# Performance work log

Hardware: AMD Instinct MI355X
Metric: run time of the kernel (lower is better)

The kernel has to match this reference:

```python
import jax, jax.numpy as jnp
import numpy as np

V, NLAB, NLAYERS, DI, DM, DS, DD, K = 32000, 9, 2, 768, 1536, 16, 96, 4
B, S = 2, 2048
EPS = 1e-6


def setup_inputs() -> dict:
    key = jax.random.key(0)
    ks = jax.random.split(key, 12)
    n = lambda k, shape, s=0.02: jax.random.normal(k, shape, jnp.float32) * s
    return {
        "input_ids": jax.random.randint(ks[0], (B, S), 0, V, dtype=jnp.int32),
        "attention_mask": jnp.ones((B, S), jnp.int32),
        "emb": n(ks[1], (V, DI)),
        "norm_w": jnp.ones((NLAYERS, DI), jnp.float32),
        "in_proj_w": n(ks[2], (NLAYERS, 2 * DM, DI)),
        "conv_w": n(ks[3], (NLAYERS, DM, K), 0.1),
        "conv_b": jnp.zeros((NLAYERS, DM), jnp.float32),
        "sB_w": n(ks[4], (NLAYERS, DS, DM)),
        "sC_w": n(ks[5], (NLAYERS, DS, DM)),
        "sD1_w": n(ks[6], (NLAYERS, DD, DM)),
        "sD2_w": n(ks[7], (NLAYERS, DM, DD)),
        "A": jnp.tile(jnp.arange(1, DS + 1, dtype=jnp.float32), (NLAYERS, DM, 1)),
        "Dp": jnp.ones((NLAYERS, DM), jnp.float32),
        "out_w": n(ks[8], (NLAYERS, DI, DM)),
        "cls_w": n(ks[9], (NLAB, DI)),
        "cls_b": jnp.zeros((NLAB,), jnp.float32),
    }


def _rmsnorm(x, w):
    return x * jax.lax.rsqrt(jnp.mean(x * x, axis=-1, keepdims=True) + EPS) * w


def _mamba_block(x, norm_w, Wi, cw, cb, WB, WC, W1, W2, A, Dp, Wo):
    # x: (b, l, d_input)
    h = _rmsnorm(x, norm_w)
    a, gate = jnp.split(h @ Wi.T, 2, axis=-1)  # each (b, l, DM)
    # causal depthwise conv1d, kernel K, left-pad K-1 (== Conv1d(pad=K-1)[..., :l])
    L = a.shape[1]
    ap = jnp.pad(a, ((0, 0), (K - 1, 0), (0, 0)))
    conv = cb + sum(ap[:, i:i + L, :] * cw[:, i] for i in range(K))
    a = jax.nn.silu(conv)
    # selective SSM
    Bm = a @ WB.T                                   # (b, l, DS)
    Cm = a @ WC.T                                   # (b, l, DS)
    delta = jax.nn.softplus(Dp + (a @ W1.T) @ W2.T)  # (b, l, DM)
    A_bar = jnp.exp(delta[..., None] * (-A))         # (b, l, DM, DS)
    X_bar = (delta * a)[..., None] * Bm[:, :, None, :]  # (b, l, DM, DS)

    def comb(c1, c2):
        a1, x1 = c1
        a2, x2 = c2
        return a1 * a2, a2 * x1 + x2

    _, hid = jax.lax.associative_scan(comb, (A_bar, X_bar), axis=1)
    y = jnp.einsum('blds,bls->bld', hid, Cm) + Dp * a
    y = y * jax.nn.silu(gate)
    return y @ Wo.T


def _forward(input_ids, attention_mask, emb, norm_w, in_proj_w, conv_w, conv_b,
             sB_w, sC_w, sD1_w, sD2_w, A, Dp, out_w, cls_w, cls_b):
    x = emb[input_ids] * attention_mask[..., None].astype(emb.dtype)
    for i in range(NLAYERS):  # residual Mamba layers
        x = _mamba_block(x, norm_w[i], in_proj_w[i], conv_w[i], conv_b[i],
                         sB_w[i], sC_w[i], sD1_w[i], sD2_w[i], A[i], Dp[i], out_w[i]) + x
    # dropout is identity at inference
    return x @ cls_w.T + cls_b  # logits (b, l, num_labels)


def reference(input_ids, attention_mask, emb, norm_w, in_proj_w, conv_w, conv_b,
              sB_w, sC_w, sD1_w, sD2_w, A, Dp, out_w, cls_w, cls_b):
    return _forward(input_ids, attention_mask, emb, norm_w, in_proj_w, conv_w, conv_b,
                    sB_w, sC_w, sD1_w, sD2_w, A, Dp, out_w, cls_w, cls_b)
```

## Files before the change

### kernel.cpp

```cpp
#include <hip/hip_runtime.h>
#include <hip/hip_bf16.h>
#include <math.h>

#define NLAB 9
#define NL   2
#define DI   768
#define DM   1536
#define DS   16
#define KC   4
#define DD   96
#define BB   2
#define SS   2048
#define TT   (BB*SS)
#define EPSF 1e-6f

#define NCH  64
#define CL   (SS/NCH)

#define NW   128
#define KS   8
#define KSL  (DM/KS)

typedef __attribute__((ext_vector_type(4))) float f32x4;
typedef __attribute__((ext_vector_type(8))) short bf16x8;
typedef __attribute__((ext_vector_type(4))) unsigned short us4;

__device__ __forceinline__ float siluf(float x) { return x / (1.f + __expf(-x)); }
__device__ __forceinline__ float softplusf(float x) { return x > 15.f ? x : log1pf(__expf(x)); }

__device__ __forceinline__ unsigned short f2bf(float f) {
    unsigned u = __float_as_uint(f);
    return (unsigned short)((u + 0x7fffu + ((u >> 16) & 1u)) >> 16);
}

__global__ void f32_to_bf16(const float* __restrict__ src,
                            unsigned short* __restrict__ dst, int n)
{
    int i = (blockIdx.x * 256 + threadIdx.x) * 8;
    if (i >= n) return;
    float4 a = *(const float4*)(src + i);
    float4 b = *(const float4*)(src + i + 4);
    union { unsigned short s[8]; uint4 v; } o;
    o.s[0] = f2bf(a.x); o.s[1] = f2bf(a.y); o.s[2] = f2bf(a.z); o.s[3] = f2bf(a.w);
    o.s[4] = f2bf(b.x); o.s[5] = f2bf(b.y); o.s[6] = f2bf(b.z); o.s[7] = f2bf(b.w);
    *(uint4*)(dst + i) = o.v;
}

__global__ void embed_kernel(const int* __restrict__ ids, const int* __restrict__ mask,
                             const float* __restrict__ emb, float* __restrict__ x)
{
    int t = blockIdx.x;
    int i = threadIdx.x;
    float m = (float)mask[t];
    int id = ids[t];
    float4 v = ((const float4*)(emb + (size_t)id * DI))[i];
    v.x *= m; v.y *= m; v.z *= m; v.w *= m;
    ((float4*)(x + (size_t)t * DI))[i] = v;
}

__global__ void rmsnorm_kernel(const float* __restrict__ x, const float* __restrict__ w,
                               unsigned short* __restrict__ h)
{
    __shared__ float red[4];
    int t = blockIdx.x;
    const float* xr = x + (size_t)t * DI;
    float ss = 0.f;
    for (int i = threadIdx.x; i < DI; i += 256) { float v = xr[i]; ss += v * v; }
    #pragma unroll
    for (int m = 1; m < 64; m <<= 1) ss += __shfl_xor(ss, m, 64);
    if ((threadIdx.x & 63) == 0) red[threadIdx.x >> 6] = ss;
    __syncthreads();
    float scale = rsqrtf((red[0] + red[1] + red[2] + red[3]) * (1.f / DI) + EPSF);
    for (int i = threadIdx.x; i < DI; i += 256)
        h[(size_t)t * DI + i] = f2bf(xr[i] * scale * w[i]);
}

#define STAGE_TILE(AS, BS, KT) do {                                                           \
    _Pragma("unroll")                                                                         \
    for (int it = 0; it < 2; ++it) {                                                          \
        int rbase = it * 64 + wave * 16;                                                      \
        int row = rbase + (lane >> 2);                                                        \
        int c8 = (lane & 3) * 8;                                                              \
        __builtin_amdgcn_global_load_lds(                                                     \
            (const __attribute__((address_space(1))) unsigned int*)(Arow + (size_t)row * lda + (KT) + c8), \
            (__attribute__((address_space(3))) unsigned int*)((AS) + rbase * 32), 16, 0, 0);  \
        __builtin_amdgcn_global_load_lds(                                                     \
            (const __attribute__((address_space(1))) unsigned int*)(Brow + (size_t)row * ldb + (KT) + c8), \
            (__attribute__((address_space(3))) unsigned int*)((BS) + rbase * 32), 16, 0, 0);  \
    } } while (0)

#define COMPUTE_TILE(AS, BS) do {                                                             \
    bf16x8 af[4], bfr[4];                                                                     \
    _Pragma("unroll")                                                                         \
    for (int i = 0; i < 4; ++i)                                                               \
        af[i] = *(const bf16x8*)&(AS)[(wm + i * 16 + lr) * 32 + kh * 8];                      \
    _Pragma("unroll")                                                                         \
    for (int j = 0; j < 4; ++j)                                                               \
        bfr[j] = *(const bf16x8*)&(BS)[(wn + j * 16 + lr) * 32 + kh * 8];                     \
    _Pragma("unroll")                                                                         \
    for (int i = 0; i < 4; ++i)                                                               \
        _Pragma("unroll")                                                                     \
        for (int j = 0; j < 4; ++j)                                                           \
            acc[i][j] = __builtin_amdgcn_mfma_f32_16x16x32_bf16(af[i], bfr[j], acc[i][j], 0, 0, 0); \
    } while (0)

__global__ __launch_bounds__(256) void gemm_bf16(
    const unsigned short* __restrict__ A, const unsigned short* __restrict__ B,
    const float* __restrict__ Rres, const float* __restrict__ bias,
    float* __restrict__ C, int M, int N, int K,
    int lda, int ldb, int ldc, int act, int cstride)
{
    __shared__ unsigned short As0[128 * 32];
    __shared__ unsigned short Bs0[128 * 32];
    __shared__ unsigned short As1[128 * 32];
    __shared__ unsigned short Bs1[128 * 32];
    const int tid = threadIdx.x;
    const int wave = tid >> 6, lane = tid & 63;
    const int bm = blockIdx.y * 128, bn = blockIdx.x * 128;
    const int wm = (wave >> 1) * 64, wn = (wave & 1) * 64;
    const int lr = lane & 15, kh = lane >> 4;

    f32x4 acc[4][4] = {};

    const unsigned short* Arow = A + (size_t)bm * lda;
    const unsigned short* Brow = B + (size_t)bn * ldb;

    STAGE_TILE(As0, Bs0, 0);
    __syncthreads();

    int kt = 0;
    while (true) {
        if (kt + 32 < K) STAGE_TILE(As1, Bs1, kt + 32);
        COMPUTE_TILE(As0, Bs0);
        __syncthreads();
        kt += 32;
        if (kt >= K) break;
        if (kt + 32 < K) STAGE_TILE(As0, Bs0, kt + 32);
        COMPUTE_TILE(As1, Bs1);
        __syncthreads();
        kt += 32;
        if (kt >= K) break;
    }

    #pragma unroll
    for (int i = 0; i < 4; ++i) {
        #pragma unroll
        for (int j = 0; j < 4; ++j) {
            #pragma unroll
            for (int r = 0; r < 4; ++r) {
                int row = bm + wm + i * 16 + kh * 4 + r;
                int col = bn + wn + j * 16 + lr;
                float v = acc[i][j][r];
                if (bias) v += bias[col];
                if (act == 1) v = softplusf(v);
                if (Rres) v += Rres[(size_t)row * ldc + col];
                C[((size_t)row * ldc + col) * cstride] = v;
            }
        }
    }
}

__global__ __launch_bounds__(256) void gemm_skinny_bf16(
    const unsigned short* __restrict__ A, const unsigned short* __restrict__ B,
    float* __restrict__ Part)
{
    __shared__ unsigned short As0[128 * 32];
    __shared__ unsigned short Bs0[128 * 32];
    __shared__ unsigned short As1[128 * 32];
    __shared__ unsigned short Bs1[128 * 32];
    const int tid = threadIdx.x;
    const int wave = tid >> 6, lane = tid & 63;
    const int bm = blockIdx.x * 128;
    const int ks = blockIdx.y;
    const int k0 = ks * KSL;
    const int wm = (wave >> 1) * 64, wn = (wave & 1) * 64;
    const int lr = lane & 15, kh = lane >> 4;
    const int lda = DM, ldb = DM;

    f32x4 acc[4][4] = {};

    const unsigned short* Arow = A + (size_t)bm * DM;
    const unsigned short* Brow = B;

    STAGE_TILE(As0, Bs0, k0);
    __syncthreads();

    int kt = 0;
    while (true) {
        if (kt + 32 < KSL) STAGE_TILE(As1, Bs1, k0 + kt + 32);
        COMPUTE_TILE(As0, Bs0);
        __syncthreads();
        kt += 32;
        if (kt >= KSL) break;
        if (kt + 32 < KSL) STAGE_TILE(As0, Bs0, k0 + kt + 32);
        COMPUTE_TILE(As1, Bs1);
        __syncthreads();
        kt += 32;
        if (kt >= KSL) break;
    }

    float* out = Part + (size_t)ks * TT * NW;
    #pragma unroll
    for (int i = 0; i < 4; ++i) {
        #pragma unroll
        for (int j = 0; j < 4; ++j) {
            #pragma unroll
            for (int r = 0; r < 4; ++r) {
                int row = bm + wm + i * 16 + kh * 4 + r;
                int col = wn + j * 16 + lr;
                out[(size_t)row * NW + col] = acc[i][j][r];
            }
        }
    }
}

__global__ void skinny_reduce(const float* __restrict__ Part,
                              float* __restrict__ BCD, unsigned short* __restrict__ dd16)
{
    int idx = blockIdx.x * 256 + threadIdx.x;
    float s = 0.f;
    #pragma unroll
    for (int ks = 0; ks < KS; ++ks)
        s += Part[(size_t)ks * TT * NW + idx];
    BCD[idx] = s;
    int col = idx & (NW - 1);
    if (col >= 32)
        dd16[(size_t)(idx >> 7) * DD + (col - 32)] = f2bf(s);
}

__global__ void conv_silu_kernel(const float* __restrict__ proj, const float* __restrict__ cw,
                                 const float* __restrict__ cb, float* __restrict__ av,
                                 unsigned short* __restrict__ aconv16)
{
    int t = blockIdx.x;
    int d = blockIdx.y * 256 + threadIdx.x;
    int p = t & (SS - 1);
    float acc = cb[d];
    #pragma unroll
    for (int j = 0; j < KC; ++j) {
        int pp = p - (KC - 1) + j;
        if (pp >= 0)
            acc += cw[d * KC + j] * proj[(size_t)(t - (KC - 1) + j) * (2 * DM) + d];
    }
    float v = siluf(acc);
    av[(size_t)t * DM + d] = v;
    aconv16[(size_t)t * DM + d] = f2bf(v);
}

__global__ void concat_w_kernel(const float* __restrict__ WB, const float* __restrict__ WC,
                                const float* __restrict__ W1, unsigned short* __restrict__ Wcat16)
{
    int l = blockIdx.y;
    int row = blockIdx.x;
    const float* src;
    if (row < 16)      src = WB + (size_t)l * DS * DM + (size_t)row * DM;
    else if (row < 32) src = WC + (size_t)l * DS * DM + (size_t)(row - 16) * DM;
    else               src = W1 + (size_t)l * DD * DM + (size_t)(row - 32) * DM;
    unsigned short* dst = Wcat16 + ((size_t)l * NW + row) * DM;
    for (int i = threadIdx.x; i < DM / 4; i += 256) {
        float4 v = ((const float4*)src)[i];
        us4 u = { f2bf(v.x), f2bf(v.y), f2bf(v.z), f2bf(v.w) };
        *(us4*)(dst + i * 4) = u;
    }
}

__global__ __launch_bounds__(256) void scan_pass1(
    const float* __restrict__ dtv, const float* __restrict__ av,
    const float* __restrict__ BCD, const float* __restrict__ Amat,
    float2* __restrict__ PQ)
{
    __shared__ float4 sB4[CL][DS / 4];
    int b = blockIdx.z, c = blockIdx.y;
    int d = blockIdx.x * 256 + threadIdx.x;
    size_t rowbase = (size_t)b * SS + (size_t)c * CL;

    for (int i = threadIdx.x; i < CL * DS; i += 256)
        ((float*)sB4)[i] = BCD[(rowbase + (i >> 4)) * NW + (i & 15)];
    __syncthreads();

    float negA[DS], hid[DS];
    #pragma unroll
    for (int s = 0; s < DS; ++s) {
        negA[s] = -Amat[(size_t)d * DS + s];
        hid[s] = 0.f;
    }
    float cum = 0.f;

    const float* pd = dtv + rowbase * DM + d;
    const float* pa = av  + rowbase * DM + d;
    for (int t = 0; t < CL; ++t) {
        float dt = pd[(size_t)t * DM];
        float avv = pa[(size_t)t * DM];
        cum += dt;
        float xv = dt * avv;
        #pragma unroll
        for (int j = 0; j < DS / 4; ++j) {
            float4 bv = sB4[t][j];
            hid[4*j+0] = __expf(dt * negA[4*j+0]) * hid[4*j+0] + xv * bv.x;
            hid[4*j+1] = __expf(dt * negA[4*j+1]) * hid[4*j+1] + xv * bv.y;
            hid[4*j+2] = __expf(dt * negA[4*j+2]) * hid[4*j+2] + xv * bv.z;
            hid[4*j+3] = __expf(dt * negA[4*j+3]) * hid[4*j+3] + xv * bv.w;
        }
    }
    float2* out = PQ + ((size_t)(b * NCH + c) * DM + d) * DS;
    #pragma unroll
    for (int s = 0; s < DS; ++s)
        out[s] = make_float2(__expf(cum * negA[s]), hid[s]);
}

__global__ void scan_carry(float2* __restrict__ PQ)
{
    int idx = blockIdx.x * 256 + threadIdx.x;
    int b = idx / (DM * DS);
    int r = idx - b * (DM * DS);
    float carry = 0.f;
    for (int c = 0; c < NCH; ++c) {
        size_t o = (size_t)(b * NCH + c) * (DM * DS) + r;
        float2 pq = PQ[o];
        PQ[o].x = carry;
        carry = pq.x * carry + pq.y;
    }
}

__global__ __launch_bounds__(256) void scan_pass2(
    const float* __restrict__ dtv, const float* __restrict__ av,
    const float* __restrict__ BCD,
    const float* __restrict__ proj, const float* __restrict__ Amat,
    const float* __restrict__ Dp, const float2* __restrict__ PQ,
    unsigned short* __restrict__ y)
{
    __shared__ float4 sB4[CL][DS / 4];
    __shared__ float4 sC4[CL][DS / 4];
    int b = blockIdx.z, c = blockIdx.y;
    int d = blockIdx.x * 256 + threadIdx.x;
    size_t rowbase = (size_t)b * SS + (size_t)c * CL;

    for (int i = threadIdx.x; i < CL * DS; i += 256) {
        size_t row = rowbase + (i >> 4);
        ((float*)sB4)[i] = BCD[row * NW + (i & 15)];
        ((float*)sC4)[i] = BCD[row * NW + 16 + (i & 15)];
    }
    __syncthreads();

    float negA[DS], hid[DS];
    const float2* pin = PQ + ((size_t)(b * NCH + c) * DM + d) * DS;
    #pragma unroll
    for (int s = 0; s < DS; ++s) {
        negA[s] = -Amat[(size_t)d * DS + s];
        hid[s] = pin[s].x;
    }
    float Dpd = Dp[d];

    const float* pd = dtv + rowbase * DM + d;
    const float* pa = av  + rowbase * DM + d;
    const float* gp = proj + rowbase * (2 * DM) + DM + d;
    unsigned short* yp = y + rowbase * DM + d;

    for (int t = 0; t < CL; ++t) {
        float dt = pd[(size_t)t * DM];
        float avv = pa[(size_t)t * DM];
        float g  = gp[(size_t)t * (2 * DM)];
        float xv = dt * avv;
        float acc0 = 0.f, acc1 = 0.f, acc2 = 0.f, acc3 = 0.f;
        #pragma unroll
        for (int j = 0; j < DS / 4; ++j) {
            float4 bv = sB4[t][j];
            float4 cv = sC4[t][j];
            hid[4*j+0] = __expf(dt * negA[4*j+0]) * hid[4*j+0] + xv * bv.x;
            hid[4*j+1] = __expf(dt * negA[4*j+1]) * hid[4*j+1] + xv * bv.y;
            hid[4*j+2] = __expf(dt * negA[4*j+2]) * hid[4*j+2] + xv * bv.z;
            hid[4*j+3] = __expf(dt * negA[4*j+3]) * hid[4*j+3] + xv * bv.w;
            acc0 += hid[4*j+0] * cv.x;
            acc1 += hid[4*j+1] * cv.y;
            acc2 += hid[4*j+2] * cv.z;
            acc3 += hid[4*j+3] * cv.w;
        }
        float contrib = (acc0 + acc1) + (acc2 + acc3);
        yp[(size_t)t * DM] = f2bf((contrib + Dpd * avv) * siluf(g));
    }
}

__global__ void cls_kernel(const float* __restrict__ x, const float* __restrict__ W,
                           const float* __restrict__ bias, float* __restrict__ out)
{
    int t = blockIdx.x;
    int lane = threadIdx.x;
    const float* xr = x + (size_t)t * DI;
    float acc[NLAB];
    #pragma unroll
    for (int n = 0; n < NLAB; ++n) acc[n] = 0.f;
    for (int i = lane; i < DI; i += 64) {
        float xv = xr[i];
        #pragma unroll
        for (int n = 0; n < NLAB; ++n) acc[n] += xv * W[(size_t)n * DI + i];
    }
    #pragma unroll
    for (int n = 0; n < NLAB; ++n)
        #pragma unroll
        for (int m = 1; m < 64; m <<= 1) acc[n] += __shfl_xor(acc[n], m, 64);
    if (lane < NLAB) out[(size_t)t * NLAB + lane] = acc[lane] + bias[lane];
}

extern "C" void kernel_launch(void* const* d_in, const int* in_sizes, int n_in,
                              void* d_out, int out_size, void* d_ws, size_t ws_size,
                              hipStream_t stream)
{
    const int*   ids    = (const int*)d_in[0];
    const int*   mask   = (const int*)d_in[1];
    const float* emb    = (const float*)d_in[2];
    const float* norm_w = (const float*)d_in[3];
    const float* Wi     = (const float*)d_in[4];
    const float* conv_w = (const float*)d_in[5];
    const float* conv_b = (const float*)d_in[6];
    const float* sB_w   = (const float*)d_in[7];
    const float* sC_w   = (const float*)d_in[8];
    const float* sD1_w  = (const float*)d_in[9];
    const float* sD2_w  = (const float*)d_in[10];
    const float* Amat   = (const float*)d_in[11];
    const float* Dp     = (const float*)d_in[12];
    const float* out_w  = (const float*)d_in[13];
    const float* cls_w  = (const float*)d_in[14];
    const float* cls_b  = (const float*)d_in[15];
    float* logits = (float*)d_out;

    float* ws = (float*)d_ws;
    size_t off = 0;
    float* x     = ws + off; off += (size_t)TT * DI;
    float* proj  = ws + off; off += (size_t)TT * 2 * DM;
    float* dtv   = ws + off; off += (size_t)TT * DM;
    float* av    = ws + off; off += (size_t)TT * DM;
    float* BCD   = ws + off; off += (size_t)TT * NW;
    size_t scratch_sz = (size_t)BB * NCH * DM * DS * 2;
    size_t part_sz = (size_t)KS * TT * NW;
    if (part_sz > scratch_sz) scratch_sz = part_sz;
    float* Part  = ws + off;
    float2* PQ   = (float2*)(ws + off); off += scratch_sz;
    unsigned short* y16     = (unsigned short*)(ws + off); off += (size_t)TT * DM / 2;
    unsigned short* aconv16 = (unsigned short*)(ws + off); off += (size_t)TT * DM / 2;
    unsigned short* Wi16    = (unsigned short*)(ws + off); off += (size_t)NL * 2 * DM * DI / 2;
    unsigned short* Wo16    = (unsigned short*)(ws + off); off += (size_t)NL * DI * DM / 2;
    unsigned short* W216    = (unsigned short*)(ws + off); off += (size_t)NL * DM * DD / 2;
    unsigned short* dd16    = (unsigned short*)(ws + off); off += (size_t)TT * DD / 2;
    unsigned short* Wcat16  = (unsigned short*)(ws + off); off += (size_t)NL * NW * DM / 2;
    if (ws_size < off * sizeof(float)) return;

    unsigned short* h16 = (unsigned short*)dtv;

    embed_kernel<<<TT, DI / 4, 0, stream>>>(ids, mask, emb, x);
    concat_w_kernel<<<dim3(NW, NL), 256, 0, stream>>>(sB_w, sC_w, sD1_w, Wcat16);

    f32_to_bf16<<<(NL * 2 * DM * DI / 8 + 255) / 256, 256, 0, stream>>>(Wi, Wi16, NL * 2 * DM * DI);
    f32_to_bf16<<<(NL * DI * DM / 8 + 255) / 256, 256, 0, stream>>>(out_w, Wo16, NL * DI * DM);
    f32_to_bf16<<<(NL * DM * DD / 8 + 255) / 256, 256, 0, stream>>>(sD2_w, W216, NL * DM * DD);

    for (int l = 0; l < NL; ++l) {
        const float* cw_l  = conv_w + (size_t)l * DM * KC;
        const float* cb_l  = conv_b + (size_t)l * DM;
        const float* A_l   = Amat  + (size_t)l * DM * DS;
        const float* Dp_l  = Dp    + (size_t)l * DM;
        const float* nw_l  = norm_w + (size_t)l * DI;
        const unsigned short* Wi16_l  = Wi16  + (size_t)l * 2 * DM * DI;
        const unsigned short* Wo16_l  = Wo16  + (size_t)l * DI * DM;
        const unsigned short* W216_l  = W216  + (size_t)l * DM * DD;
        const unsigned short* Wcat16_l = Wcat16 + (size_t)l * NW * DM;

        rmsnorm_kernel<<<TT, 256, 0, stream>>>(x, nw_l, h16);

        gemm_bf16<<<dim3(2 * DM / 128, TT / 128), 256, 0, stream>>>(
            h16, Wi16_l, nullptr, nullptr, proj, TT, 2 * DM, DI, DI, DI, 2 * DM, 0, 1);

        conv_silu_kernel<<<dim3(TT, DM / 256), 256, 0, stream>>>(proj, cw_l, cb_l, av, aconv16);

        gemm_skinny_bf16<<<dim3(TT / 128, KS), 256, 0, stream>>>(aconv16, Wcat16_l, Part);
        skinny_reduce<<<TT * NW / 256, 256, 0, stream>>>(Part, BCD, dd16);

        gemm_bf16<<<dim3(DM / 128, TT / 128), 256, 0, stream>>>(
            dd16, W216_l, nullptr, Dp_l, dtv, TT, DM, DD, DD, DD, DM, 1, 1);

        scan_pass1<<<dim3(DM / 256, NCH, BB), 256, 0, stream>>>(dtv, av, BCD, A_l, PQ);
        scan_carry<<<BB * DM * DS / 256, 256, 0, stream>>>(PQ);
        scan_pass2<<<dim3(DM / 256, NCH, BB), 256, 0, stream>>>(
            dtv, av, BCD, proj, A_l, Dp_l, PQ, y16);

        gemm_bf16<<<dim3(DI / 128, TT / 128), 256, 0, stream>>>(
            y16, Wo16_l, x, nullptr, x, TT, DI, DM, DM, DM, DI, 0, 1);
    }

    cls_kernel<<<TT, 64, 0, stream>>>(x, cls_w, cls_b, logits);
}
```

Measured before the change: 753.7 us.

## Triple-buffer GEMM LDS pipeline with swizzle, vmcnt waits, and block remapping

Both bf16 GEMM kernels move from double to triple LDS buffering. Full __syncthreads are replaced with s_waitcnt vmcnt(4) plus a raw barrier, so two tile loads stay in flight while MFMA compute runs. An XOR swizzle on the k-chunk offset, applied the same way at store and load, is meant to cut LDS bank conflicts on the fragment reads. The main GEMM also remaps block IDs across groups of 8 for better L2 locality, and the carry-scan loop gets an unroll hint. The cost is 50% more LDS per block, which can reduce occupancy, and the vmcnt counts are hand-tuned against the issued load count.

```diff
diff --git a/kernel.cpp b/kernel.cpp
--- a/kernel.cpp
+++ b/kernel.cpp
@@ -80,7 +80,7 @@
     for (int it = 0; it < 2; ++it) {                                                          \
         int rbase = it * 64 + wave * 16;                                                      \
         int row = rbase + (lane >> 2);                                                        \
-        int c8 = (lane & 3) * 8;                                                              \
+        int c8 = (((lane & 3) ^ ((lane >> 3) & 3)) * 8);                                      \
         __builtin_amdgcn_global_load_lds(                                                     \
             (const __attribute__((address_space(1))) unsigned int*)(Arow + (size_t)row * lda + (KT) + c8), \
             (__attribute__((address_space(3))) unsigned int*)((AS) + rbase * 32), 16, 0, 0);  \
@@ -91,12 +91,13 @@
 
 #define COMPUTE_TILE(AS, BS) do {                                                             \
     bf16x8 af[4], bfr[4];                                                                     \
+    const int khs = (kh ^ ((lr >> 1) & 3)) * 8;                                               \
     _Pragma("unroll")                                                                         \
     for (int i = 0; i < 4; ++i)                                                               \
-        af[i] = *(const bf16x8*)&(AS)[(wm + i * 16 + lr) * 32 + kh * 8];                      \
+        af[i] = *(const bf16x8*)&(AS)[(wm + i * 16 + lr) * 32 + khs];                         \
     _Pragma("unroll")                                                                         \
     for (int j = 0; j < 4; ++j)                                                               \
-        bfr[j] = *(const bf16x8*)&(BS)[(wn + j * 16 + lr) * 32 + kh * 8];                     \
+        bfr[j] = *(const bf16x8*)&(BS)[(wn + j * 16 + lr) * 32 + khs];                        \
     _Pragma("unroll")                                                                         \
     for (int i = 0; i < 4; ++i)                                                               \
         _Pragma("unroll")                                                                     \
@@ -104,6 +105,12 @@
             acc[i][j] = __builtin_amdgcn_mfma_f32_16x16x32_bf16(af[i], bfr[j], acc[i][j], 0, 0, 0); \
     } while (0)
 
+#define WAIT_BAR(T, NT) do {                                                                  \
+    if ((T) + 1 < (NT)) asm volatile("s_waitcnt vmcnt(4)" ::: "memory");                      \
+    else                asm volatile("s_waitcnt vmcnt(0)" ::: "memory");                      \
+    __builtin_amdgcn_s_barrier();                                                             \
+} while (0)
+
 __global__ __launch_bounds__(256) void gemm_bf16(
     const unsigned short* __restrict__ A, const unsigned short* __restrict__ B,
     const float* __restrict__ Rres, const float* __restrict__ bias,
@@ -114,9 +121,17 @@
     __shared__ unsigned short Bs0[128 * 32];
     __shared__ unsigned short As1[128 * 32];
     __shared__ unsigned short Bs1[128 * 32];
+    __shared__ unsigned short As2[128 * 32];
+    __shared__ unsigned short Bs2[128 * 32];
     const int tid = threadIdx.x;
     const int wave = tid >> 6, lane = tid & 63;
-    const int bm = blockIdx.y * 128, bn = blockIdx.x * 128;
+
+    const int nwg = gridDim.x * gridDim.y;
+    int flat = blockIdx.y * gridDim.x + blockIdx.x;
+    int nf = (flat & 7) * (nwg >> 3) + (flat >> 3);
+    const int bm = (nf / gridDim.x) * 128;
+    const int bn = (nf % gridDim.x) * 128;
+
     const int wm = (wave >> 1) * 64, wn = (wave & 1) * 64;
     const int lr = lane & 15, kh = lane >> 4;
 
@@ -125,21 +140,24 @@
     const unsigned short* Arow = A + (size_t)bm * lda;
     const unsigned short* Brow = B + (size_t)bn * ldb;
 
+    const int nt = K >> 5;
     STAGE_TILE(As0, Bs0, 0);
-    __syncthreads();
-
-    int kt = 0;
+    if (nt > 1) STAGE_TILE(As1, Bs1, 32);
+
+    int t = 0;
     while (true) {
-        if (kt + 32 < K) STAGE_TILE(As1, Bs1, kt + 32);
+        WAIT_BAR(t, nt);
+        if (t + 2 < nt) STAGE_TILE(As2, Bs2, (t + 2) * 32);
         COMPUTE_TILE(As0, Bs0);
-        __syncthreads();
-        kt += 32;
-        if (kt >= K) break;
-        if (kt + 32 < K) STAGE_TILE(As0, Bs0, kt + 32);
+        if (++t == nt) break;
+        WAIT_BAR(t, nt);
+        if (t + 2 < nt) STAGE_TILE(As0, Bs0, (t + 2) * 32);
         COMPUTE_TILE(As1, Bs1);
-        __syncthreads();
-        kt += 32;
-        if (kt >= K) break;
+        if (++t == nt) break;
+        WAIT_BAR(t, nt);
+        if (t + 2 < nt) STAGE_TILE(As1, Bs1, (t + 2) * 32);
+        COMPUTE_TILE(As2, Bs2);
+        if (++t == nt) break;
     }
 
     #pragma unroll
@@ -168,6 +186,8 @@
     __shared__ unsigned short Bs0[128 * 32];
     __shared__ unsigned short As1[128 * 32];
     __shared__ unsigned short Bs1[128 * 32];
+    __shared__ unsigned short As2[128 * 32];
+    __shared__ unsigned short Bs2[128 * 32];
     const int tid = threadIdx.x;
     const int wave = tid >> 6, lane = tid & 63;
     const int bm = blockIdx.x * 128;
@@ -182,21 +202,24 @@
     const unsigned short* Arow = A + (size_t)bm * DM;
     const unsigned short* Brow = B;
 
+    const int nt = KSL >> 5;
     STAGE_TILE(As0, Bs0, k0);
-    __syncthreads();
-
-    int kt = 0;
+    STAGE_TILE(As1, Bs1, k0 + 32);
+
+    int t = 0;
     while (true) {
-        if (kt + 32 < KSL) STAGE_TILE(As1, Bs1, k0 + kt + 32);
+        WAIT_BAR(t, nt);
+        if (t + 2 < nt) STAGE_TILE(As2, Bs2, k0 + (t + 2) * 32);
         COMPUTE_TILE(As0, Bs0);
-        __syncthreads();
-        kt += 32;
-        if (kt >= KSL) break;
-        if (kt + 32 < KSL) STAGE_TILE(As0, Bs0, k0 + kt + 32);
+        if (++t == nt) break;
+        WAIT_BAR(t, nt);
+        if (t + 2 < nt) STAGE_TILE(As0, Bs0, k0 + (t + 2) * 32);
         COMPUTE_TILE(As1, Bs1);
-        __syncthreads();
-        kt += 32;
-        if (kt >= KSL) break;
+        if (++t == nt) break;
+        WAIT_BAR(t, nt);
+        if (t + 2 < nt) STAGE_TILE(As1, Bs1, k0 + (t + 2) * 32);
+        COMPUTE_TILE(As2, Bs2);
+        if (++t == nt) break;
     }
 
     float* out = Part + (size_t)ks * TT * NW;
@@ -314,6 +337,7 @@
     int b = idx / (DM * DS);
     int r = idx - b * (DM * DS);
     float carry = 0.f;
+    #pragma unroll 4
     for (int c = 0; c < NCH; ++c) {
         size_t o = (size_t)(b * NCH + c) * (DM * DS) + r;
         float2 pq = PQ[o];
```

After: 731.6 us. 2.9% less time.
